# Kernel optimization log

Hardware: AMD Instinct MI355X
Metric: run time of the kernel (lower is better)

Reference implementation:

```python
import math
import jax, jax.numpy as jnp
import numpy as np

B, T, C = 2, 2048, 2048
H, G = 16, 4          # n_head, n_group
HKV = H // G          # kv heads
HD = C // H           # head dim = 128

def setup_inputs() -> dict:
    key = jax.random.key(0)
    ks = jax.random.split(key, 4)
    s = 0.02  # realistic init scale
    return {
        "x": jax.random.normal(ks[0], (B, T, C), jnp.float32),
        "Wkv": jax.random.normal(ks[1], (C, 2 * C // G), jnp.float32) * s,
        "bkv": jnp.zeros((2 * C // G,), jnp.float32),
        "Wq": jax.random.normal(ks[2], (C, C), jnp.float32) * s,
        "bq": jnp.zeros((C,), jnp.float32),
        "Wp": jax.random.normal(ks[3], (C, C), jnp.float32) * s,
        "bp": jnp.zeros((C,), jnp.float32),
    }

def _expand_kv(t):
    # (B,T,HKV*HD) -> replicate each kv head G times -> (B,H,T,HD)
    t = t.reshape(B, T, HKV, HD)
    t = jnp.broadcast_to(t[:, :, None], (B, T, G, HKV, HD)).reshape(B, T, H, HD)
    return t.transpose(0, 2, 1, 3)

def reference(x, Wkv, bkv, Wq, bq, Wp, bp):
    kv = x @ Wkv + bkv                      # (B,T,2C/G)
    k, v = jnp.split(kv, 2, axis=-1)
    q = (x @ Wq + bq).reshape(B, T, H, HD).transpose(0, 2, 1, 3)  # (B,H,T,HD)
    k = _expand_kv(k)
    v = _expand_kv(v)
    att = jnp.einsum('bhqd,bhkd->bhqk', q, k) * (1.0 / math.sqrt(HD))
    mask = jnp.tril(jnp.ones((T, T), bool))
    att = jnp.where(mask, att, -jnp.inf)
    att = jax.nn.softmax(att, axis=-1)
    y = jnp.einsum('bhqk,bhkd->bhqd', att, v)
    y = y.transpose(0, 2, 1, 3).reshape(B, T, C)
    return y @ Wp + bp
```

## Files before the change

### kernel.cpp

```cpp
#include <hip/hip_runtime.h>

#define Bv 2
#define Tv 2048
#define Cv 2048
#define Hv 16
#define HKVv 4
#define HDv 128

typedef __attribute__((ext_vector_type(8))) __bf16 bf16x8;
typedef __attribute__((ext_vector_type(4))) float floatx4;

__device__ __forceinline__ unsigned short f2b(float f) {
  unsigned int x = __float_as_uint(f);
  x += 0x7fffu + ((x >> 16) & 1u);
  return (unsigned short)(x >> 16);
}

#define MFMA(a, b, c) __builtin_amdgcn_mfma_f32_16x16x32_bf16((a), (b), (c), 0, 0, 0)

__device__ __forceinline__ void gld_lds16(const void* g, void* l) {
  __builtin_amdgcn_global_load_lds((const __attribute__((address_space(1))) void*)g,
                                   (__attribute__((address_space(3))) void*)l, 16, 0, 0);
}

__global__ __launch_bounds__(256) void prep_kernel(
    const float* __restrict__ x, unsigned short* __restrict__ xb,
    const float* __restrict__ Wq, unsigned short* __restrict__ wq_t,
    const float* __restrict__ Wkv, unsigned short* __restrict__ wkv_t,
    const float* __restrict__ Wp, unsigned short* __restrict__ wp_t) {
  __shared__ float tile[32][33];
  int bid = blockIdx.x, tid = threadIdx.x;
  if (bid < 8192) {
    int i = bid * 256 + tid;
    float4 f = ((const float4*)x)[i];
    ushort4 u;
    u.x = f2b(f.x); u.y = f2b(f.y); u.z = f2b(f.z); u.w = f2b(f.w);
    ((ushort4*)xb)[i] = u;
    return;
  }
  const float* src; unsigned short* dst; int N, idx;
  if (bid < 8192 + 4096)      { idx = bid - 8192;  src = Wq;  dst = wq_t;  N = 2048; }
  else if (bid < 8192 + 6144) { idx = bid - 12288; src = Wkv; dst = wkv_t; N = 1024; }
  else                        { idx = bid - 14336; src = Wp;  dst = wp_t;  N = 2048; }
  const int K = 2048;
  int k0 = (idx & 63) * 32, n0 = (idx >> 6) * 32;
  int tx = tid & 31, ty = tid >> 5;
  for (int i = ty; i < 32; i += 8)
    tile[i][tx] = src[(size_t)(k0 + i) * N + n0 + tx];
  __syncthreads();
  for (int i = ty; i < 32; i += 8)
    dst[(size_t)(n0 + i) * K + k0 + tx] = f2b(tile[tx][i]);
}

__global__ __launch_bounds__(256) void gemm_qkv(
    const unsigned short* __restrict__ xb,
    const unsigned short* __restrict__ wq_t,
    const unsigned short* __restrict__ wkv_t,
    const float* __restrict__ bq, const float* __restrict__ bkv,
    unsigned short* __restrict__ qs,
    unsigned short* __restrict__ ks,
    unsigned short* __restrict__ vs) {
  __shared__ __align__(16) unsigned short Ash[2][128 * 32];
  __shared__ __align__(16) unsigned short Bsh[2][128 * 32];
  int tid = threadIdx.x;
  int wave = tid >> 6, lane = tid & 63;
  int c = lane & 15, quad = lane >> 4;
  int wr = (wave >> 1) * 64, wc = (wave & 1) * 64;
  int m0 = blockIdx.x * 128, n0 = blockIdx.y * 128;
  bool isq = (n0 < 2048);
  const unsigned short* wt = isq ? (wq_t + (size_t)n0 * 2048)
                                 : (wkv_t + (size_t)(n0 - 2048) * 2048);
  floatx4 zero4 = {0.f, 0.f, 0.f, 0.f};
  floatx4 acc[4][4];
#pragma unroll
  for (int i = 0; i < 4; i++)
#pragma unroll
    for (int j = 0; j < 4; j++) acc[i][j] = zero4;

  const unsigned short* Abase = xb + (size_t)m0 * 2048;
  int s0 = wave * 128 + lane, s1 = wave * 128 + 64 + lane;
  int r0 = s0 >> 2, kc0 = (s0 & 3) ^ ((r0 >> 1) & 3);
  int r1 = s1 >> 2, kc1 = (s1 & 3) ^ ((r1 >> 1) & 3);
  int swz3 = quad ^ ((c >> 1) & 3);
  int dA0 = (wave * 128) * 8, dA1 = (wave * 128 + 64) * 8;

  gld_lds16(Abase + (size_t)r0 * 2048 + kc0 * 8, &Ash[0][0] + dA0);
  gld_lds16(Abase + (size_t)r1 * 2048 + kc1 * 8, &Ash[0][0] + dA1);
  gld_lds16(wt + (size_t)r0 * 2048 + kc0 * 8, &Bsh[0][0] + dA0);
  gld_lds16(wt + (size_t)r1 * 2048 + kc1 * 8, &Bsh[0][0] + dA1);
  __syncthreads();

  for (int it = 0; it < 64; it++) {
    int cur = it & 1;
    if (it + 1 < 64) {
      int k1 = (it + 1) * 32;
      gld_lds16(Abase + (size_t)r0 * 2048 + k1 + kc0 * 8, &Ash[cur ^ 1][0] + dA0);
      gld_lds16(Abase + (size_t)r1 * 2048 + k1 + kc1 * 8, &Ash[cur ^ 1][0] + dA1);
      gld_lds16(wt + (size_t)r0 * 2048 + k1 + kc0 * 8, &Bsh[cur ^ 1][0] + dA0);
      gld_lds16(wt + (size_t)r1 * 2048 + k1 + kc1 * 8, &Bsh[cur ^ 1][0] + dA1);
    }
    bf16x8 af[4], bfv[4];
#pragma unroll
    for (int i = 0; i < 4; i++)
      af[i] = *(const bf16x8*)(&Ash[cur][(wr + i * 16 + c) * 32 + swz3 * 8]);
#pragma unroll
    for (int j = 0; j < 4; j++)
      bfv[j] = *(const bf16x8*)(&Bsh[cur][(wc + j * 16 + c) * 32 + swz3 * 8]);
#pragma unroll
    for (int i = 0; i < 4; i++)
#pragma unroll
      for (int j = 0; j < 4; j++)
        acc[i][j] = MFMA(af[i], bfv[j], acc[i][j]);
    __syncthreads();
  }

#pragma unroll
  for (int i = 0; i < 4; i++) {
#pragma unroll
    for (int j = 0; j < 4; j++) {
#pragma unroll
      for (int r = 0; r < 4; r++) {
        int m = m0 + wr + i * 16 + quad * 4 + r;
        int n = n0 + wc + j * 16 + c;
        int bidx = m >> 11, t = m & 2047;
        float val = acc[i][j][r];
        if (isq) {
          val = (val + bq[n]) * 0.08838834764831845f;
          int hh = n >> 7, d = n & 127;
          qs[((size_t)((bidx * Hv + hh) * Tv) + t) * HDv + d] = f2b(val);
        } else {
          int n2 = n - 2048;
          val += bkv[n2];
          if (n2 < 512) {
            int hh = n2 >> 7, d = n2 & 127;
            ks[((size_t)((bidx * HKVv + hh) * Tv) + t) * HDv + d] = f2b(val);
          } else {
            int n3 = n2 - 512;
            int hh = n3 >> 7, d = n3 & 127;
            vs[((size_t)((bidx * HKVv + hh) * HDv) + d) * Tv + t] = f2b(val);
          }
        }
      }
    }
  }
}

__global__ __launch_bounds__(256, 4) void attn_kernel(
    const unsigned short* __restrict__ qs,
    const unsigned short* __restrict__ ks,
    const unsigned short* __restrict__ vs,
    unsigned short* __restrict__ ys) {
  __shared__ __align__(16) unsigned short Ksh[2][32 * 128];
  __shared__ __align__(16) unsigned short Vsh[2][128 * 32];
  __shared__ __align__(16) unsigned short Psh[4][16 * 32];

  int id = blockIdx.x;
  int g = id & 7, r = id >> 3;
  int t = r & 31, hh = r >> 5;
  int qt = (t & 1) ? (31 - (t >> 1)) : (t >> 1);
  int b = g >> 2, hkv = g & 3;
  int h = hh * 4 + hkv;
  int tid = threadIdx.x;
  int wave = tid >> 6, lane = tid & 63;
  int c = lane & 15, quad = lane >> 4;
  int q0w = qt * 64 + wave * 16;
  int qrow = q0w + c;
  int swzK = c & 7, swzV = (c >> 1) & 3;

  const unsigned short* qptr = qs + ((size_t)((b * Hv + h) * Tv) + q0w) * HDv;
  const unsigned short* kbase = ks + (size_t)((b * HKVv + hkv) * Tv) * HDv;
  const unsigned short* vbase = vs + (size_t)((b * HKVv + hkv) * HDv) * Tv;

  bf16x8 qf[4];
#pragma unroll
  for (int kc = 0; kc < 4; kc++)
    qf[kc] = *(const bf16x8*)(qptr + (size_t)c * HDv + kc * 32 + quad * 8);

  floatx4 zero4 = {0.f, 0.f, 0.f, 0.f};
  floatx4 o[8];
#pragma unroll
  for (int dt = 0; dt < 8; dt++) o[dt] = zero4;
  float M = -1e30f, L = 0.f;

  unsigned short* Pw = &Psh[wave][0];

  int kOff[2], vOff[2];
#pragma unroll
  for (int i = 0; i < 2; i++) {
    int s = wave * 128 + i * 64 + lane;
    int rk = s >> 4, gk = (s & 15) ^ (rk & 7);
    kOff[i] = rk * 128 + gk * 8;
    int rv = s >> 2, gv = (s & 3) ^ ((rv >> 1) & 3);
    vOff[i] = rv * Tv + gv * 8;
  }
  int ldsBase = (wave * 128) * 8;

  int ntiles = 2 * qt + 2;

#pragma unroll
  for (int i = 0; i < 2; i++) gld_lds16(kbase + kOff[i], &Ksh[0][0] + ldsBase + i * 512);
#pragma unroll
  for (int i = 0; i < 2; i++) gld_lds16(vbase + vOff[i], &Vsh[0][0] + ldsBase + i * 512);
  __syncthreads();

  for (int kt = 0; kt < ntiles; kt++) {
    int kv0 = kt * 32;
    int cur = kt & 1;
    if (kt + 1 < ntiles) {
      int kv1 = (kt + 1) * 32;
#pragma unroll
      for (int i = 0; i < 2; i++)
        gld_lds16(kbase + (size_t)kv1 * 128 + kOff[i], &Ksh[cur ^ 1][0] + ldsBase + i * 512);
#pragma unroll
      for (int i = 0; i < 2; i++)
        gld_lds16(vbase + kv1 + vOff[i], &Vsh[cur ^ 1][0] + ldsBase + i * 512);
    }

    if (kv0 <= q0w + 15) {
      const unsigned short* Kb = &Ksh[cur][0];
      const unsigned short* Vb = &Vsh[cur][0];
      floatx4 st[2] = {zero4, zero4};
#pragma unroll
      for (int kc = 0; kc < 4; kc++) {
#pragma unroll
        for (int sub = 0; sub < 2; sub++) {
          bf16x8 kf = *(const bf16x8*)(&Kb[(sub * 16 + c) * 128 + (((kc * 4 + quad) ^ swzK) * 8)]);
          st[sub] = MFMA(kf, qf[kc], st[sub]);
        }
      }
      if (kv0 + 31 > q0w) {
#pragma unroll
        for (int sub = 0; sub < 2; sub++) {
          int kvb = kv0 + sub * 16 + quad * 4;
#pragma unroll
          for (int r2 = 0; r2 < 4; r2++)
            if (kvb + r2 > qrow) st[sub][r2] = -1e30f;
        }
      }
      float mx = -1e30f;
#pragma unroll
      for (int sub = 0; sub < 2; sub++)
        mx = fmaxf(mx, fmaxf(fmaxf(st[sub][0], st[sub][1]), fmaxf(st[sub][2], st[sub][3])));
      mx = fmaxf(mx, __shfl_xor(mx, 16));
      mx = fmaxf(mx, __shfl_xor(mx, 32));
      if (!__all(mx <= M + 8.0f)) {
        float Mn = fmaxf(M, mx);
        float al = __expf(M - Mn);
        M = Mn;
        L *= al;
#pragma unroll
        for (int dt = 0; dt < 8; dt++) o[dt] *= al;
      }
      float l = 0.f;
#pragma unroll
      for (int sub = 0; sub < 2; sub++) {
        float p0 = __expf(st[sub][0] - M);
        float p1 = __expf(st[sub][1] - M);
        float p2 = __expf(st[sub][2] - M);
        float p3 = __expf(st[sub][3] - M);
        l += (p0 + p1) + (p2 + p3);
        unsigned int lo = (unsigned int)f2b(p0) | ((unsigned int)f2b(p1) << 16);
        unsigned int hi = (unsigned int)f2b(p2) | ((unsigned int)f2b(p3) << 16);
        int gg = (sub * 2 + (quad >> 1)) ^ swzV;
        *(uint2*)(&Pw[c * 32 + gg * 8 + (quad & 1) * 4]) = make_uint2(lo, hi);
      }
      l += __shfl_xor(l, 16);
      l += __shfl_xor(l, 32);
      L += l;
      bf16x8 pf = *(const bf16x8*)(&Pw[c * 32 + ((quad ^ swzV) * 8)]);
#pragma unroll
      for (int dt = 0; dt < 8; dt++) {
        bf16x8 vf = *(const bf16x8*)(&Vb[(dt * 16 + c) * 32 + ((quad ^ swzV) * 8)]);
        o[dt] = MFMA(vf, pf, o[dt]);
      }
    }
    __syncthreads();
  }

  float Li = 1.0f / L;
  size_t rowbase = ((size_t)(b * Tv + qrow)) * Cv + h * HDv;
#pragma unroll
  for (int dt = 0; dt < 8; dt++) {
    unsigned int lo = (unsigned int)f2b(o[dt][0] * Li) | ((unsigned int)f2b(o[dt][1] * Li) << 16);
    unsigned int hi2 = (unsigned int)f2b(o[dt][2] * Li) | ((unsigned int)f2b(o[dt][3] * Li) << 16);
    *(uint2*)(&ys[rowbase + dt * 16 + quad * 4]) = make_uint2(lo, hi2);
  }
}

__global__ __launch_bounds__(256) void gemm_proj(
    const unsigned short* __restrict__ ys,
    const unsigned short* __restrict__ wp_t,
    const float* __restrict__ bp,
    float* __restrict__ out) {
  __shared__ __align__(16) unsigned short Ash[2][128 * 32];
  __shared__ __align__(16) unsigned short Bsh[2][128 * 32];
  int tid = threadIdx.x;
  int wave = tid >> 6, lane = tid & 63;
  int c = lane & 15, quad = lane >> 4;
  int wr = (wave >> 1) * 64, wc = (wave & 1) * 64;
  int m0 = blockIdx.x * 128, n0 = blockIdx.y * 128;
  floatx4 zero4 = {0.f, 0.f, 0.f, 0.f};
  floatx4 acc[4][4];
#pragma unroll
  for (int i = 0; i < 4; i++)
#pragma unroll
    for (int j = 0; j < 4; j++) acc[i][j] = zero4;

  const unsigned short* Abase = ys + (size_t)m0 * 2048;
  const unsigned short* Bbase = wp_t + (size_t)n0 * 2048;
  int s0 = wave * 128 + lane, s1 = wave * 128 + 64 + lane;
  int r0 = s0 >> 2, kc0 = (s0 & 3) ^ ((r0 >> 1) & 3);
  int r1 = s1 >> 2, kc1 = (s1 & 3) ^ ((r1 >> 1) & 3);
  int swz3 = quad ^ ((c >> 1) & 3);
  int dA0 = (wave * 128) * 8, dA1 = (wave * 128 + 64) * 8;

  gld_lds16(Abase + (size_t)r0 * 2048 + kc0 * 8, &Ash[0][0] + dA0);
  gld_lds16(Abase + (size_t)r1 * 2048 + kc1 * 8, &Ash[0][0] + dA1);
  gld_lds16(Bbase + (size_t)r0 * 2048 + kc0 * 8, &Bsh[0][0] + dA0);
  gld_lds16(Bbase + (size_t)r1 * 2048 + kc1 * 8, &Bsh[0][0] + dA1);
  __syncthreads();

  for (int it = 0; it < 64; it++) {
    int cur = it & 1;
    if (it + 1 < 64) {
      int k1 = (it + 1) * 32;
      gld_lds16(Abase + (size_t)r0 * 2048 + k1 + kc0 * 8, &Ash[cur ^ 1][0] + dA0);
      gld_lds16(Abase + (size_t)r1 * 2048 + k1 + kc1 * 8, &Ash[cur ^ 1][0] + dA1);
      gld_lds16(Bbase + (size_t)r0 * 2048 + k1 + kc0 * 8, &Bsh[cur ^ 1][0] + dA0);
      gld_lds16(Bbase + (size_t)r1 * 2048 + k1 + kc1 * 8, &Bsh[cur ^ 1][0] + dA1);
    }
    bf16x8 af[4], bfv[4];
#pragma unroll
    for (int i = 0; i < 4; i++)
      af[i] = *(const bf16x8*)(&Ash[cur][(wr + i * 16 + c) * 32 + swz3 * 8]);
#pragma unroll
    for (int j = 0; j < 4; j++)
      bfv[j] = *(const bf16x8*)(&Bsh[cur][(wc + j * 16 + c) * 32 + swz3 * 8]);
#pragma unroll
    for (int i = 0; i < 4; i++)
#pragma unroll
      for (int j = 0; j < 4; j++)
        acc[i][j] = MFMA(af[i], bfv[j], acc[i][j]);
    __syncthreads();
  }

#pragma unroll
  for (int i = 0; i < 4; i++) {
#pragma unroll
    for (int j = 0; j < 4; j++) {
#pragma unroll
      for (int r = 0; r < 4; r++) {
        int m = m0 + wr + i * 16 + quad * 4 + r;
        int n = n0 + wc + j * 16 + c;
        out[(size_t)m * 2048 + n] = acc[i][j][r] + bp[n];
      }
    }
  }
}

extern "C" void kernel_launch(void* const* d_in, const int* in_sizes, int n_in,
                              void* d_out, int out_size, void* d_ws, size_t ws_size,
                              hipStream_t stream) {
  (void)in_sizes; (void)n_in; (void)out_size; (void)ws_size;
  const float* x   = (const float*)d_in[0];
  const float* Wkv = (const float*)d_in[1];
  const float* bkv = (const float*)d_in[2];
  const float* Wq  = (const float*)d_in[3];
  const float* bq  = (const float*)d_in[4];
  const float* Wp  = (const float*)d_in[5];
  const float* bp  = (const float*)d_in[6];
  float* out = (float*)d_out;

  char* ws = (char*)d_ws;
  unsigned short* xb    = (unsigned short*)(ws + 0);
  unsigned short* wq_t  = (unsigned short*)(ws + 16777216);
  unsigned short* wkv_t = (unsigned short*)(ws + 25165824);
  unsigned short* wp_t  = (unsigned short*)(ws + 29360128);
  unsigned short* qs    = (unsigned short*)(ws + 37748736);
  unsigned short* ks    = (unsigned short*)(ws + 54525952);
  unsigned short* vs    = (unsigned short*)(ws + 58720256);
  unsigned short* ysbuf = (unsigned short*)(ws + 62914560);

  prep_kernel<<<18432, 256, 0, stream>>>(x, xb, Wq, wq_t, Wkv, wkv_t, Wp, wp_t);
  gemm_qkv<<<dim3(32, 24), 256, 0, stream>>>(xb, wq_t, wkv_t, bq, bkv, qs, ks, vs);
  attn_kernel<<<1024, 256, 0, stream>>>(qs, ks, vs, ysbuf);
  gemm_proj<<<dim3(32, 16), 256, 0, stream>>>(ysbuf, wp_t, bp, out);
}
```

Baseline: 367.7 us.

## Remap GEMM tiles per XCD, shuffle P in registers, and regrid attention

Both GEMMs remap block indices so that blocks on the same XCD share contiguous M/N tile ranges, aiming for better L2 reuse. The attention kernel drops the per-wave LDS staging of softmax probabilities and builds the MFMA B operand through cross-lane shuffles instead. The attention kernel also switches to a 3D grid with head-parity-based causal load balancing and asks for 5 blocks per CU. The shuffles add ALU work and the higher occupancy target may pressure registers.

```diff
diff --git a/kernel.cpp b/kernel.cpp
--- a/kernel.cpp
+++ b/kernel.cpp
@@ -14,6 +14,10 @@
   unsigned int x = __float_as_uint(f);
   x += 0x7fffu + ((x >> 16) & 1u);
   return (unsigned short)(x >> 16);
+}
+
+__device__ __forceinline__ unsigned int pk2(float a, float b) {
+  return (unsigned int)f2b(a) | ((unsigned int)f2b(b) << 16);
 }
 
 #define MFMA(a, b, c) __builtin_amdgcn_mfma_f32_16x16x32_bf16((a), (b), (c), 0, 0, 0)
@@ -66,7 +70,11 @@
   int wave = tid >> 6, lane = tid & 63;
   int c = lane & 15, quad = lane >> 4;
   int wr = (wave >> 1) * 64, wc = (wave & 1) * 64;
-  int m0 = blockIdx.x * 128, n0 = blockIdx.y * 128;
+  int fid = blockIdx.y * gridDim.x + blockIdx.x;
+  int xcd = fid & 7, u = fid >> 3;
+  int mr = u & 7, nr = u >> 3;
+  int m0 = ((xcd & 3) * 8 + mr) * 128;
+  int n0 = ((xcd >> 2) * 12 + nr) * 128;
   bool isq = (n0 < 2048);
   const unsigned short* wt = isq ? (wq_t + (size_t)n0 * 2048)
                                  : (wkv_t + (size_t)(n0 - 2048) * 2048);
@@ -145,27 +153,23 @@
   }
 }
 
-__global__ __launch_bounds__(256, 4) void attn_kernel(
+__global__ __launch_bounds__(256, 5) void attn_kernel(
     const unsigned short* __restrict__ qs,
     const unsigned short* __restrict__ ks,
     const unsigned short* __restrict__ vs,
     unsigned short* __restrict__ ys) {
   __shared__ __align__(16) unsigned short Ksh[2][32 * 128];
   __shared__ __align__(16) unsigned short Vsh[2][128 * 32];
-  __shared__ __align__(16) unsigned short Psh[4][16 * 32];
-
-  int id = blockIdx.x;
-  int g = id & 7, r = id >> 3;
-  int t = r & 31, hh = r >> 5;
-  int qt = (t & 1) ? (31 - (t >> 1)) : (t >> 1);
-  int b = g >> 2, hkv = g & 3;
-  int h = hh * 4 + hkv;
+
+  int x = blockIdx.x, h = blockIdx.y, b = blockIdx.z;
+  int qt = (h & 8) ? (31 - x) : x;
+  int hkv = h & (HKVv - 1);
   int tid = threadIdx.x;
   int wave = tid >> 6, lane = tid & 63;
   int c = lane & 15, quad = lane >> 4;
   int q0w = qt * 64 + wave * 16;
   int qrow = q0w + c;
-  int swzK = c & 7, swzV = (c >> 1) & 3;
+  int swzK = c & 7;
 
   const unsigned short* qptr = qs + ((size_t)((b * Hv + h) * Tv) + q0w) * HDv;
   const unsigned short* kbase = ks + (size_t)((b * HKVv + hkv) * Tv) * HDv;
@@ -181,8 +185,6 @@
 #pragma unroll
   for (int dt = 0; dt < 8; dt++) o[dt] = zero4;
   float M = -1e30f, L = 0.f;
-
-  unsigned short* Pw = &Psh[wave][0];
 
   int kOff[2], vOff[2];
 #pragma unroll
@@ -196,6 +198,8 @@
   int ldsBase = (wave * 128) * 8;
 
   int ntiles = 2 * qt + 2;
+  int swzV = (c >> 1) & 3;
+  bool doswap = (quad == 1) || (quad == 2);
 
 #pragma unroll
   for (int i = 0; i < 2; i++) gld_lds16(kbase + kOff[i], &Ksh[0][0] + ldsBase + i * 512);
@@ -251,23 +255,26 @@
 #pragma unroll
         for (int dt = 0; dt < 8; dt++) o[dt] *= al;
       }
-      float l = 0.f;
-#pragma unroll
-      for (int sub = 0; sub < 2; sub++) {
-        float p0 = __expf(st[sub][0] - M);
-        float p1 = __expf(st[sub][1] - M);
-        float p2 = __expf(st[sub][2] - M);
-        float p3 = __expf(st[sub][3] - M);
-        l += (p0 + p1) + (p2 + p3);
-        unsigned int lo = (unsigned int)f2b(p0) | ((unsigned int)f2b(p1) << 16);
-        unsigned int hi = (unsigned int)f2b(p2) | ((unsigned int)f2b(p3) << 16);
-        int gg = (sub * 2 + (quad >> 1)) ^ swzV;
-        *(uint2*)(&Pw[c * 32 + gg * 8 + (quad & 1) * 4]) = make_uint2(lo, hi);
-      }
+      float p00 = __expf(st[0][0] - M), p01 = __expf(st[0][1] - M);
+      float p02 = __expf(st[0][2] - M), p03 = __expf(st[0][3] - M);
+      float p10 = __expf(st[1][0] - M), p11 = __expf(st[1][1] - M);
+      float p12 = __expf(st[1][2] - M), p13 = __expf(st[1][3] - M);
+      float l = ((p00 + p01) + (p02 + p03)) + ((p10 + p11) + (p12 + p13));
       l += __shfl_xor(l, 16);
       l += __shfl_xor(l, 32);
       L += l;
-      bf16x8 pf = *(const bf16x8*)(&Pw[c * 32 + ((quad ^ swzV) * 8)]);
+      unsigned int W00 = pk2(p00, p01), W01 = pk2(p02, p03);
+      unsigned int W10 = pk2(p10, p11), W11 = pk2(p12, p13);
+      unsigned int t00 = __shfl_xor(W00, 16), t01 = __shfl_xor(W01, 16);
+      unsigned int t10 = __shfl_xor(W10, 16), t11 = __shfl_xor(W11, 16);
+      unsigned int X0, X1, X2, X3;
+      if ((quad & 1) == 0) { X0 = W00; X1 = W01; X2 = t00; X3 = t01; }
+      else                 { X0 = t10; X1 = t11; X2 = W10; X3 = W11; }
+      unsigned int y0 = __shfl_xor(X0, 48), y1 = __shfl_xor(X1, 48);
+      unsigned int y2 = __shfl_xor(X2, 48), y3 = __shfl_xor(X3, 48);
+      if (doswap) { X0 = y0; X1 = y1; X2 = y2; X3 = y3; }
+      unsigned int pw[4] = {X0, X1, X2, X3};
+      bf16x8 pf = *(const bf16x8*)pw;
 #pragma unroll
       for (int dt = 0; dt < 8; dt++) {
         bf16x8 vf = *(const bf16x8*)(&Vb[(dt * 16 + c) * 32 + ((quad ^ swzV) * 8)]);
@@ -298,7 +305,11 @@
   int wave = tid >> 6, lane = tid & 63;
   int c = lane & 15, quad = lane >> 4;
   int wr = (wave >> 1) * 64, wc = (wave & 1) * 64;
-  int m0 = blockIdx.x * 128, n0 = blockIdx.y * 128;
+  int fid = blockIdx.y * gridDim.x + blockIdx.x;
+  int xcd = fid & 7, u = fid >> 3;
+  int mr = u & 7, nr = u >> 3;
+  int m0 = ((xcd & 3) * 8 + mr) * 128;
+  int n0 = ((xcd >> 2) * 8 + nr) * 128;
   floatx4 zero4 = {0.f, 0.f, 0.f, 0.f};
   floatx4 acc[4][4];
 #pragma unroll
@@ -383,6 +394,6 @@
 
   prep_kernel<<<18432, 256, 0, stream>>>(x, xb, Wq, wq_t, Wkv, wkv_t, Wp, wp_t);
   gemm_qkv<<<dim3(32, 24), 256, 0, stream>>>(xb, wq_t, wkv_t, bq, bkv, qs, ks, vs);
-  attn_kernel<<<1024, 256, 0, stream>>>(qs, ks, vs, ysbuf);
+  attn_kernel<<<dim3(32, 16, 2), 256, 0, stream>>>(qs, ks, vs, ysbuf);
   gemm_proj<<<dim3(32, 16), 256, 0, stream>>>(ysbuf, wp_t, bp, out);
 }
```

Result: faster. 343.4 us (-6.6%).
